# Optimization experiments

Measured on AMD Instinct MI355X. Metric: run time of the kernel, lower is better.

## Reference

```python
import jax, jax.numpy as jnp
import numpy as np

B, V, H, W = 2, 4, 352, 352
R_PIX = H * W
SH_DEGREE = 1
D_SH = (SH_DEGREE + 1) ** 2
SCALE_MIN, SCALE_MAX = 0.5, 15.0
EPS = 1e-8
C0 = 0.28209479177387814  # SH DC basis constant


def quat_to_mat(q):
    # (w, x, y, z) convention, matches pytorch3d quaternion_to_matrix
    w, x, y, z = q[..., 0], q[..., 1], q[..., 2], q[..., 3]
    two_s = 2.0 / jnp.sum(q * q, axis=-1)
    o = jnp.stack([
        1 - two_s * (y * y + z * z), two_s * (x * y - z * w), two_s * (x * z + y * w),
        two_s * (x * y + z * w), 1 - two_s * (x * x + z * z), two_s * (y * z - x * w),
        two_s * (x * z - y * w), two_s * (y * z + x * w), 1 - two_s * (x * x + y * y),
    ], axis=-1)
    return o.reshape(*q.shape[:-1], 3, 3)


def setup_inputs() -> dict:
    key = jax.random.key(0)
    ks = jax.random.split(key, 8)
    # valid c2w extrinsics: random rotation (from unit quaternion) + translation
    q = jax.random.normal(ks[0], (B, V, 4))
    q = q / jnp.linalg.norm(q, axis=-1, keepdims=True)
    Rm = quat_to_mat(q)
    t = jax.random.normal(ks[1], (B, V, 3))
    E = jnp.zeros((B, V, 4, 4))
    E = E.at[..., :3, :3].set(Rm).at[..., :3, 3].set(t).at[..., 3, 3].set(1.0)
    extrinsics = E.reshape(B, V, 1, 1, 1, 4, 4)
    # normalized pinhole intrinsics
    f = jax.random.uniform(ks[2], (B, V, 2), minval=0.8, maxval=1.2)
    K = jnp.zeros((B, V, 3, 3))
    K = K.at[..., 0, 0].set(f[..., 0]).at[..., 1, 1].set(f[..., 1])
    K = K.at[..., 0, 2].set(0.5).at[..., 1, 2].set(0.5).at[..., 2, 2].set(1.0)
    intrinsics = K.reshape(B, V, 1, 1, 1, 3, 3)
    coordinates = jax.random.uniform(ks[3], (B, V, R_PIX, 1, 1, 2))
    depths = jax.random.uniform(ks[4], (B, V, R_PIX, 1, 1), minval=0.5, maxval=10.0)
    opacities = jax.random.uniform(ks[5], (B, V, R_PIX, 1, 1))
    raw_gaussians = jax.random.normal(ks[6], (B, V, R_PIX, 1, 1, 7 + 3 * D_SH))
    input_images = jax.random.uniform(ks[7], (B, V, 3, H, W))
    sh_mask = jnp.ones((D_SH,), jnp.float32)
    for deg in range(1, SH_DEGREE + 1):
        sh_mask = sh_mask.at[deg ** 2:(deg + 1) ** 2].set(0.1 * 0.25 ** deg)
    return {"extrinsics": extrinsics, "intrinsics": intrinsics, "coordinates": coordinates,
            "depths": depths, "opacities": opacities, "raw_gaussians": raw_gaussians,
            "input_images": input_images, "sh_mask": sh_mask}


def reference(extrinsics, intrinsics, coordinates, depths, opacities, raw_gaussians, input_images, sh_mask):
    d_sh = sh_mask.shape[0]
    # split raw gaussians: scales (3), quaternion (4), sh (3*d_sh)
    scales = jnp.clip(jax.nn.softplus(raw_gaussians[..., :3] - 4.0), SCALE_MIN, SCALE_MAX)
    rot = raw_gaussians[..., 3:7]
    rotations = rot / (jnp.linalg.norm(rot, axis=-1, keepdims=True) + EPS)
    sh = raw_gaussians[..., 7:].reshape(*raw_gaussians.shape[:-1], 3, d_sh) * sh_mask
    # inject image colors into the DC SH coefficient
    b, v, c, h, w = input_images.shape
    imgs = input_images.transpose(0, 1, 3, 4, 2).reshape(b, v, h * w, 1, 1, c)
    sh = sh.at[..., 0].add((imgs - 0.5) / C0)  # RGB2SH
    # covariance = R diag(s^2) R^T, then rotate into world frame
    Rq = quat_to_mat(rotations)
    cov = jnp.einsum('...ij,...j,...kj->...ik', Rq, scales * scales, Rq)
    Rc = extrinsics[..., :3, :3]  # (b,v,1,1,1,3,3) c2w rotation
    cov = jnp.einsum('...ij,...jk,...lk->...il', Rc, cov, Rc)
    # unproject rays: d = normalize(K^-1 [x,y,1]), world dir = R d, origin = t
    Kinv = jnp.linalg.inv(intrinsics)
    xy1 = jnp.concatenate([coordinates, jnp.ones_like(coordinates[..., :1])], axis=-1)
    d = jnp.einsum('...ij,...j->...i', Kinv, xy1)
    d = d / jnp.linalg.norm(d, axis=-1, keepdims=True)
    dirs = jnp.einsum('...ij,...j->...i', Rc, d)
    means = jnp.broadcast_to(extrinsics[..., :3, 3], dirs.shape) + dirs * depths[..., None]
    # rotate SH: degree 0 identity; degree 1 Wigner-D = P R P^T with P: (x,y,z)->(y,z,x)
    perm = jnp.array([1, 2, 0])
    D1 = Rc[..., perm[:, None], perm[None, :]]  # (b,v,1,1,1,3,3)
    sh1 = jnp.einsum('...ij,...xj->...xi', D1, sh[..., 1:4])
    harmonics = jnp.concatenate([sh[..., :1], sh1], axis=-1)
    return means, cov, scales, rotations, harmonics, opacities
```

## Files before the change

kernel.cpp:

```cpp
#include <hip/hip_runtime.h>


#define R_PIX 123904
#define NVIEW 8
#define NPIX  (R_PIX * (size_t)NVIEW)

#define OFF_MEANS  ((size_t)0)
#define OFF_COV    ((size_t)(3  * NPIX))
#define OFF_SCALES ((size_t)(12 * NPIX))
#define OFF_ROT    ((size_t)(15 * NPIX))
#define OFF_HARM   ((size_t)(19 * NPIX))
#define OFF_OPAC   ((size_t)(31 * NPIX))

typedef float f4v __attribute__((ext_vector_type(4)));
typedef float f4u __attribute__((ext_vector_type(4), aligned(4)));

__device__ __forceinline__ void nt_store4(float* p, float x, float y, float z, float w) {
    f4v v = { x, y, z, w };
    __builtin_nontemporal_store(v, (f4v*)p);
}

__global__ __launch_bounds__(256) void gaussian_adapter_kernel(
    const float* __restrict__ extr,
    const float* __restrict__ intr,
    const float* __restrict__ coords,
    const float* __restrict__ depths,
    const float* __restrict__ opac,
    const float* __restrict__ raw,
    const float* __restrict__ imgs,
    const float* __restrict__ shmask,
    float* __restrict__ out)
{
    const int t   = threadIdx.x;
    const int bv  = blockIdx.y;
    const int bp0 = blockIdx.x * 256;
    const size_t base_pix = (size_t)bv * R_PIX + bp0;
    const int p   = bp0 + t;
    const size_t pix = base_pix + t;

    const float* rp = raw + pix * 19;
    const f4u r0 = *(const f4u*)(rp);
    const f4u r1 = *(const f4u*)(rp + 4);
    const f4u r2 = *(const f4u*)(rp + 8);
    const f4u r3 = *(const f4u*)(rp + 12);
    const float r16 = rp[16], r17 = rp[17], r18 = rp[18];

    const float2 uv  = ((const float2*)coords)[pix];
    const float  dep = depths[pix];
    const float  op  = opac[pix];
    float im[3];
    #pragma unroll
    for (int c = 0; c < 3; c++)
        im[c] = imgs[((size_t)bv * 3 + c) * R_PIX + p];

    float Rc[3][3], tvec[3];
    {
        const float* E = extr + bv * 16;
        #pragma unroll
        for (int i = 0; i < 3; i++) {
            #pragma unroll
            for (int j = 0; j < 3; j++) Rc[i][j] = E[i * 4 + j];
            tvec[i] = E[i * 4 + 3];
        }
    }
    const float* K = intr + bv * 9;
    const float fx = K[0], cx = K[2];
    const float fy = K[4], cy = K[5];
    const float sm0 = shmask[0], sm1 = shmask[1], sm2 = shmask[2], sm3 = shmask[3];

    float rg[19] = { r0.x, r0.y, r0.z, r0.w,
                     r1.x, r1.y, r1.z, r1.w,
                     r2.x, r2.y, r2.z, r2.w,
                     r3.x, r3.y, r3.z, r3.w,
                     r16, r17, r18 };

    const float LOG2E = 1.4426950408889634f;
    const float LN2   = 0.6931471805599453f;
    float sc[3];
    #pragma unroll
    for (int k = 0; k < 3; k++) {
        float xv = rg[k] - 4.0f;
        float e  = __builtin_amdgcn_exp2f(-fabsf(xv) * LOG2E);
        float sp = fmaxf(xv, 0.0f) + LN2 * __builtin_amdgcn_logf(1.0f + e);
        sc[k] = fminf(fmaxf(sp, 0.5f), 15.0f);
    }

    float q0 = rg[3], q1 = rg[4], q2 = rg[5], q3 = rg[6];
    {
        const float qn = q0 * q0 + q1 * q1 + q2 * q2 + q3 * q3;
        const float inorm = __builtin_amdgcn_rsqf(qn);
        q0 *= inorm; q1 *= inorm; q2 *= inorm; q3 *= inorm;
    }

    const float two_s = 2.0f;
    float Rq[3][3];
    Rq[0][0] = 1.0f - two_s * (q2 * q2 + q3 * q3);
    Rq[0][1] = two_s * (q1 * q2 - q3 * q0);
    Rq[0][2] = two_s * (q1 * q3 + q2 * q0);
    Rq[1][0] = two_s * (q1 * q2 + q3 * q0);
    Rq[1][1] = 1.0f - two_s * (q1 * q1 + q3 * q3);
    Rq[1][2] = two_s * (q2 * q3 - q1 * q0);
    Rq[2][0] = two_s * (q1 * q3 - q2 * q0);
    Rq[2][1] = two_s * (q2 * q3 + q1 * q0);
    Rq[2][2] = 1.0f - two_s * (q1 * q1 + q2 * q2);

    const float s2[3] = { sc[0] * sc[0], sc[1] * sc[1], sc[2] * sc[2] };
    float cov3[3][3];
    #pragma unroll
    for (int i = 0; i < 3; i++)
        #pragma unroll
        for (int k = 0; k < 3; k++)
            cov3[i][k] = Rq[i][0] * s2[0] * Rq[k][0]
                       + Rq[i][1] * s2[1] * Rq[k][1]
                       + Rq[i][2] * s2[2] * Rq[k][2];
    float cov[3][3];
    #pragma unroll
    for (int i = 0; i < 3; i++) {
        float m0 = Rc[i][0] * cov3[0][0] + Rc[i][1] * cov3[1][0] + Rc[i][2] * cov3[2][0];
        float m1 = Rc[i][0] * cov3[0][1] + Rc[i][1] * cov3[1][1] + Rc[i][2] * cov3[2][1];
        float m2 = Rc[i][0] * cov3[0][2] + Rc[i][1] * cov3[1][2] + Rc[i][2] * cov3[2][2];
        #pragma unroll
        for (int l = 0; l < 3; l++)
            cov[i][l] = m0 * Rc[l][0] + m1 * Rc[l][1] + m2 * Rc[l][2];
    }

    float means[3];
    {
        const float rfx = __builtin_amdgcn_rcpf(fx);
        const float rfy = __builtin_amdgcn_rcpf(fy);
        float d0 = (uv.x - cx) * rfx;
        float d1 = (uv.y - cy) * rfy;
        const float rn = __builtin_amdgcn_rsqf(d0 * d0 + d1 * d1 + 1.0f);
        d0 *= rn; d1 *= rn;
        const float d2 = rn;
        #pragma unroll
        for (int i = 0; i < 3; i++)
            means[i] = tvec[i] + (Rc[i][0] * d0 + Rc[i][1] * d1 + Rc[i][2] * d2) * dep;
    }

    float harm[3][4];
    {
        const float invC0 = 1.0f / 0.28209479177387814f;
        const int perm[3] = {1, 2, 0};
        #pragma unroll
        for (int c = 0; c < 3; c++) {
            float s1  = rg[7 + c * 4 + 1] * sm1;
            float s2v = rg[7 + c * 4 + 2] * sm2;
            float s3  = rg[7 + c * 4 + 3] * sm3;
            harm[c][0] = rg[7 + c * 4] * sm0 + (im[c] - 0.5f) * invC0;
            #pragma unroll
            for (int i = 0; i < 3; i++)
                harm[c][1 + i] = Rc[perm[i]][perm[0]] * s1
                               + Rc[perm[i]][perm[1]] * s2v
                               + Rc[perm[i]][perm[2]] * s3;
        }
    }

    nt_store4(out + OFF_ROT + pix * 4, q0, q1, q2, q3);
    {
        float* g = out + OFF_HARM + pix * 12;
        nt_store4(g,     harm[0][0], harm[0][1], harm[0][2], harm[0][3]);
        nt_store4(g + 4, harm[1][0], harm[1][1], harm[1][2], harm[1][3]);
        nt_store4(g + 8, harm[2][0], harm[2][1], harm[2][2], harm[2][3]);
    }
    __builtin_nontemporal_store(op, out + OFF_OPAC + pix);

    {
        float* g = out + OFF_MEANS + pix * 3;
        #pragma unroll
        for (int i = 0; i < 3; i++) g[i] = means[i];
    }
    {
        float* g = out + OFF_COV + pix * 9;
        #pragma unroll
        for (int i = 0; i < 3; i++)
            #pragma unroll
            for (int j = 0; j < 3; j++) g[i * 3 + j] = cov[i][j];
    }
    {
        float* g = out + OFF_SCALES + pix * 3;
        #pragma unroll
        for (int i = 0; i < 3; i++) g[i] = sc[i];
    }
}

extern "C" void kernel_launch(void* const* d_in, const int* in_sizes, int n_in,
                              void* d_out, int out_size, void* d_ws, size_t ws_size,
                              hipStream_t stream) {
    const float* extr   = (const float*)d_in[0];
    const float* intr   = (const float*)d_in[1];
    const float* coords = (const float*)d_in[2];
    const float* depths = (const float*)d_in[3];
    const float* opac   = (const float*)d_in[4];
    const float* raw    = (const float*)d_in[5];
    const float* imgs   = (const float*)d_in[6];
    const float* shmask = (const float*)d_in[7];
    float* out = (float*)d_out;

    dim3 grid(R_PIX / 256, NVIEW);
    dim3 block(256);
    gaussian_adapter_kernel<<<grid, block, 0, stream>>>(
        extr, intr, coords, depths, opac, raw, imgs, shmask, out);
}
```

Baseline: 228.2 us.

## Process four pixel tiles per block with all loads batched upfront

Each block now handles four 256-pixel tiles and issues every global load for all tiles before computing, increasing memory-level parallelism per thread. Per-view constants are also loaded once per four pixels. The cost is higher register pressure, possibly lower occupancy, and fewer blocks in the grid.

```diff
diff --git a/kernel.cpp b/kernel.cpp
--- a/kernel.cpp
+++ b/kernel.cpp
@@ -4,6 +4,9 @@
 #define R_PIX 123904
 #define NVIEW 8
 #define NPIX  (R_PIX * (size_t)NVIEW)
+#define TILES 4
+
+static_assert(R_PIX % (256 * TILES) == 0, "tile cover");
 
 #define OFF_MEANS  ((size_t)0)
 #define OFF_COV    ((size_t)(3  * NPIX))
@@ -33,25 +36,8 @@
 {
     const int t   = threadIdx.x;
     const int bv  = blockIdx.y;
-    const int bp0 = blockIdx.x * 256;
-    const size_t base_pix = (size_t)bv * R_PIX + bp0;
-    const int p   = bp0 + t;
-    const size_t pix = base_pix + t;
-
-    const float* rp = raw + pix * 19;
-    const f4u r0 = *(const f4u*)(rp);
-    const f4u r1 = *(const f4u*)(rp + 4);
-    const f4u r2 = *(const f4u*)(rp + 8);
-    const f4u r3 = *(const f4u*)(rp + 12);
-    const float r16 = rp[16], r17 = rp[17], r18 = rp[18];
-
-    const float2 uv  = ((const float2*)coords)[pix];
-    const float  dep = depths[pix];
-    const float  op  = opac[pix];
-    float im[3];
-    #pragma unroll
-    for (int c = 0; c < 3; c++)
-        im[c] = imgs[((size_t)bv * 3 + c) * R_PIX + p];
+    const int bp0 = blockIdx.x * (256 * TILES);
+    const size_t base = (size_t)bv * R_PIX + bp0;
 
     float Rc[3][3], tvec[3];
     {
@@ -68,119 +54,146 @@
     const float fy = K[4], cy = K[5];
     const float sm0 = shmask[0], sm1 = shmask[1], sm2 = shmask[2], sm3 = shmask[3];
 
-    float rg[19] = { r0.x, r0.y, r0.z, r0.w,
-                     r1.x, r1.y, r1.z, r1.w,
-                     r2.x, r2.y, r2.z, r2.w,
-                     r3.x, r3.y, r3.z, r3.w,
-                     r16, r17, r18 };
+    f4u   r0[TILES], r1[TILES], r2[TILES], r3[TILES];
+    float r16[TILES], r17[TILES], r18[TILES];
+    float2 uv[TILES];
+    float dep[TILES], op[TILES];
+    float im[TILES][3];
+    #pragma unroll
+    for (int k = 0; k < TILES; k++) {
+        const size_t pix = base + k * 256 + t;
+        const float* rp = raw + pix * 19;
+        r0[k] = *(const f4u*)(rp);
+        r1[k] = *(const f4u*)(rp + 4);
+        r2[k] = *(const f4u*)(rp + 8);
+        r3[k] = *(const f4u*)(rp + 12);
+        r16[k] = rp[16]; r17[k] = rp[17]; r18[k] = rp[18];
+        uv[k]  = ((const float2*)coords)[pix];
+        dep[k] = depths[pix];
+        op[k]  = opac[pix];
+        #pragma unroll
+        for (int c = 0; c < 3; c++)
+            im[k][c] = imgs[((size_t)bv * 3 + c) * R_PIX + bp0 + k * 256 + t];
+    }
 
     const float LOG2E = 1.4426950408889634f;
     const float LN2   = 0.6931471805599453f;
-    float sc[3];
+    const float invC0 = 1.0f / 0.28209479177387814f;
+    const float rfx = __builtin_amdgcn_rcpf(fx);
+    const float rfy = __builtin_amdgcn_rcpf(fy);
+
     #pragma unroll
-    for (int k = 0; k < 3; k++) {
-        float xv = rg[k] - 4.0f;
-        float e  = __builtin_amdgcn_exp2f(-fabsf(xv) * LOG2E);
-        float sp = fmaxf(xv, 0.0f) + LN2 * __builtin_amdgcn_logf(1.0f + e);
-        sc[k] = fminf(fmaxf(sp, 0.5f), 15.0f);
-    }
-
-    float q0 = rg[3], q1 = rg[4], q2 = rg[5], q3 = rg[6];
-    {
-        const float qn = q0 * q0 + q1 * q1 + q2 * q2 + q3 * q3;
-        const float inorm = __builtin_amdgcn_rsqf(qn);
-        q0 *= inorm; q1 *= inorm; q2 *= inorm; q3 *= inorm;
-    }
-
-    const float two_s = 2.0f;
-    float Rq[3][3];
-    Rq[0][0] = 1.0f - two_s * (q2 * q2 + q3 * q3);
-    Rq[0][1] = two_s * (q1 * q2 - q3 * q0);
-    Rq[0][2] = two_s * (q1 * q3 + q2 * q0);
-    Rq[1][0] = two_s * (q1 * q2 + q3 * q0);
-    Rq[1][1] = 1.0f - two_s * (q1 * q1 + q3 * q3);
-    Rq[1][2] = two_s * (q2 * q3 - q1 * q0);
-    Rq[2][0] = two_s * (q1 * q3 - q2 * q0);
-    Rq[2][1] = two_s * (q2 * q3 + q1 * q0);
-    Rq[2][2] = 1.0f - two_s * (q1 * q1 + q2 * q2);
-
-    const float s2[3] = { sc[0] * sc[0], sc[1] * sc[1], sc[2] * sc[2] };
-    float cov3[3][3];
-    #pragma unroll
-    for (int i = 0; i < 3; i++)
-        #pragma unroll
-        for (int k = 0; k < 3; k++)
-            cov3[i][k] = Rq[i][0] * s2[0] * Rq[k][0]
-                       + Rq[i][1] * s2[1] * Rq[k][1]
-                       + Rq[i][2] * s2[2] * Rq[k][2];
-    float cov[3][3];
-    #pragma unroll
-    for (int i = 0; i < 3; i++) {
-        float m0 = Rc[i][0] * cov3[0][0] + Rc[i][1] * cov3[1][0] + Rc[i][2] * cov3[2][0];
-        float m1 = Rc[i][0] * cov3[0][1] + Rc[i][1] * cov3[1][1] + Rc[i][2] * cov3[2][1];
-        float m2 = Rc[i][0] * cov3[0][2] + Rc[i][1] * cov3[1][2] + Rc[i][2] * cov3[2][2];
-        #pragma unroll
-        for (int l = 0; l < 3; l++)
-            cov[i][l] = m0 * Rc[l][0] + m1 * Rc[l][1] + m2 * Rc[l][2];
-    }
-
-    float means[3];
-    {
-        const float rfx = __builtin_amdgcn_rcpf(fx);
-        const float rfy = __builtin_amdgcn_rcpf(fy);
-        float d0 = (uv.x - cx) * rfx;
-        float d1 = (uv.y - cy) * rfy;
-        const float rn = __builtin_amdgcn_rsqf(d0 * d0 + d1 * d1 + 1.0f);
-        d0 *= rn; d1 *= rn;
-        const float d2 = rn;
+    for (int k = 0; k < TILES; k++) {
+        const size_t pix = base + k * 256 + t;
+
+        float rg[19] = { r0[k].x, r0[k].y, r0[k].z, r0[k].w,
+                         r1[k].x, r1[k].y, r1[k].z, r1[k].w,
+                         r2[k].x, r2[k].y, r2[k].z, r2[k].w,
+                         r3[k].x, r3[k].y, r3[k].z, r3[k].w,
+                         r16[k], r17[k], r18[k] };
+
+        float sc[3];
+        #pragma unroll
+        for (int j = 0; j < 3; j++) {
+            float xv = rg[j] - 4.0f;
+            float e  = __builtin_amdgcn_exp2f(-fabsf(xv) * LOG2E);
+            float sp = fmaxf(xv, 0.0f) + LN2 * __builtin_amdgcn_logf(1.0f + e);
+            sc[j] = fminf(fmaxf(sp, 0.5f), 15.0f);
+        }
+
+        float q0 = rg[3], q1 = rg[4], q2 = rg[5], q3 = rg[6];
+        {
+            const float qn = q0 * q0 + q1 * q1 + q2 * q2 + q3 * q3;
+            const float inorm = __builtin_amdgcn_rsqf(qn);
+            q0 *= inorm; q1 *= inorm; q2 *= inorm; q3 *= inorm;
+        }
+
+        const float two_s = 2.0f;
+        float Rq[3][3];
+        Rq[0][0] = 1.0f - two_s * (q2 * q2 + q3 * q3);
+        Rq[0][1] = two_s * (q1 * q2 - q3 * q0);
+        Rq[0][2] = two_s * (q1 * q3 + q2 * q0);
+        Rq[1][0] = two_s * (q1 * q2 + q3 * q0);
+        Rq[1][1] = 1.0f - two_s * (q1 * q1 + q3 * q3);
+        Rq[1][2] = two_s * (q2 * q3 - q1 * q0);
+        Rq[2][0] = two_s * (q1 * q3 - q2 * q0);
+        Rq[2][1] = two_s * (q2 * q3 + q1 * q0);
+        Rq[2][2] = 1.0f - two_s * (q1 * q1 + q2 * q2);
+
+        const float s2[3] = { sc[0] * sc[0], sc[1] * sc[1], sc[2] * sc[2] };
+        float cov3[3][3];
         #pragma unroll
         for (int i = 0; i < 3; i++)
-            means[i] = tvec[i] + (Rc[i][0] * d0 + Rc[i][1] * d1 + Rc[i][2] * d2) * dep;
-    }
-
-    float harm[3][4];
-    {
-        const float invC0 = 1.0f / 0.28209479177387814f;
-        const int perm[3] = {1, 2, 0};
-        #pragma unroll
-        for (int c = 0; c < 3; c++) {
-            float s1  = rg[7 + c * 4 + 1] * sm1;
-            float s2v = rg[7 + c * 4 + 2] * sm2;
-            float s3  = rg[7 + c * 4 + 3] * sm3;
-            harm[c][0] = rg[7 + c * 4] * sm0 + (im[c] - 0.5f) * invC0;
+            #pragma unroll
+            for (int j = 0; j < 3; j++)
+                cov3[i][j] = Rq[i][0] * s2[0] * Rq[j][0]
+                           + Rq[i][1] * s2[1] * Rq[j][1]
+                           + Rq[i][2] * s2[2] * Rq[j][2];
+        float cov[3][3];
+        #pragma unroll
+        for (int i = 0; i < 3; i++) {
+            float m0 = Rc[i][0] * cov3[0][0] + Rc[i][1] * cov3[1][0] + Rc[i][2] * cov3[2][0];
+            float m1 = Rc[i][0] * cov3[0][1] + Rc[i][1] * cov3[1][1] + Rc[i][2] * cov3[2][1];
+            float m2 = Rc[i][0] * cov3[0][2] + Rc[i][1] * cov3[1][2] + Rc[i][2] * cov3[2][2];
+            #pragma unroll
+            for (int l = 0; l < 3; l++)
+                cov[i][l] = m0 * Rc[l][0] + m1 * Rc[l][1] + m2 * Rc[l][2];
+        }
+
+        float means[3];
+        {
+            float d0 = (uv[k].x - cx) * rfx;
+            float d1 = (uv[k].y - cy) * rfy;
+            const float rn = __builtin_amdgcn_rsqf(d0 * d0 + d1 * d1 + 1.0f);
+            d0 *= rn; d1 *= rn;
+            const float d2 = rn;
             #pragma unroll
             for (int i = 0; i < 3; i++)
-                harm[c][1 + i] = Rc[perm[i]][perm[0]] * s1
-                               + Rc[perm[i]][perm[1]] * s2v
-                               + Rc[perm[i]][perm[2]] * s3;
-        }
-    }
-
-    nt_store4(out + OFF_ROT + pix * 4, q0, q1, q2, q3);
-    {
-        float* g = out + OFF_HARM + pix * 12;
-        nt_store4(g,     harm[0][0], harm[0][1], harm[0][2], harm[0][3]);
-        nt_store4(g + 4, harm[1][0], harm[1][1], harm[1][2], harm[1][3]);
-        nt_store4(g + 8, harm[2][0], harm[2][1], harm[2][2], harm[2][3]);
-    }
-    __builtin_nontemporal_store(op, out + OFF_OPAC + pix);
-
-    {
-        float* g = out + OFF_MEANS + pix * 3;
-        #pragma unroll
-        for (int i = 0; i < 3; i++) g[i] = means[i];
-    }
-    {
-        float* g = out + OFF_COV + pix * 9;
-        #pragma unroll
-        for (int i = 0; i < 3; i++)
-            #pragma unroll
-            for (int j = 0; j < 3; j++) g[i * 3 + j] = cov[i][j];
-    }
-    {
-        float* g = out + OFF_SCALES + pix * 3;
-        #pragma unroll
-        for (int i = 0; i < 3; i++) g[i] = sc[i];
+                means[i] = tvec[i] + (Rc[i][0] * d0 + Rc[i][1] * d1 + Rc[i][2] * d2) * dep[k];
+        }
+
+        float harm[3][4];
+        {
+            const int perm[3] = {1, 2, 0};
+            #pragma unroll
+            for (int c = 0; c < 3; c++) {
+                float s1  = rg[7 + c * 4 + 1] * sm1;
+                float s2v = rg[7 + c * 4 + 2] * sm2;
+                float s3  = rg[7 + c * 4 + 3] * sm3;
+                harm[c][0] = rg[7 + c * 4] * sm0 + (im[k][c] - 0.5f) * invC0;
+                #pragma unroll
+                for (int i = 0; i < 3; i++)
+                    harm[c][1 + i] = Rc[perm[i]][perm[0]] * s1
+                                   + Rc[perm[i]][perm[1]] * s2v
+                                   + Rc[perm[i]][perm[2]] * s3;
+            }
+        }
+
+        nt_store4(out + OFF_ROT + pix * 4, q0, q1, q2, q3);
+        {
+            float* g = out + OFF_HARM + pix * 12;
+            nt_store4(g,     harm[0][0], harm[0][1], harm[0][2], harm[0][3]);
+            nt_store4(g + 4, harm[1][0], harm[1][1], harm[1][2], harm[1][3]);
+            nt_store4(g + 8, harm[2][0], harm[2][1], harm[2][2], harm[2][3]);
+        }
+        __builtin_nontemporal_store(op[k], out + OFF_OPAC + pix);
+        {
+            float* g = out + OFF_MEANS + pix * 3;
+            #pragma unroll
+            for (int i = 0; i < 3; i++) g[i] = means[i];
+        }
+        {
+            float* g = out + OFF_COV + pix * 9;
+            #pragma unroll
+            for (int i = 0; i < 3; i++)
+                #pragma unroll
+                for (int j = 0; j < 3; j++) g[i * 3 + j] = cov[i][j];
+        }
+        {
+            float* g = out + OFF_SCALES + pix * 3;
+            #pragma unroll
+            for (int i = 0; i < 3; i++) g[i] = sc[i];
+        }
     }
 }
 
@@ -197,7 +210,7 @@
     const float* shmask = (const float*)d_in[7];
     float* out = (float*)d_out;
 
-    dim3 grid(R_PIX / 256, NVIEW);
+    dim3 grid(R_PIX / (256 * TILES), NVIEW);
     dim3 block(256);
     gaussian_adapter_kernel<<<grid, block, 0, stream>>>(
         extr, intr, coords, depths, opac, raw, imgs, shmask, out);
```

Result: slower. 243.9 us (+6.9%).
